# Kernel tuning notes

Hardware: AMD Instinct MI355X
Metric: run time of the kernel (lower is better)

Reference implementation:

```python
import jax, jax.numpy as jnp
import numpy as np

B, P, H, W, D, C = 16, 4, 32, 32, 32, 8


def setup_inputs() -> dict:
    key = jax.random.key(0)
    k1, k2 = jax.random.split(key)
    input_fmap = jax.random.normal(k1, (B, P, H, W, D, C), dtype=jnp.float32)
    # identity affine + small noise so sampled coords mostly stay in-volume
    ident = jnp.concatenate([jnp.eye(3, dtype=jnp.float32), jnp.zeros((3, 1), jnp.float32)], axis=1)
    theta = ident[None, None] + 0.05 * jax.random.normal(k2, (B, P, 3, 4), dtype=jnp.float32)
    return {"input_fmap": input_fmap, "theta": theta}


def _affine_grid(theta, H, W, D):
    # matches tf.meshgrid default 'xy' indexing: shapes (H, W, D)
    x = jnp.arange(W, dtype=jnp.float32)
    y = jnp.arange(H, dtype=jnp.float32)
    z = jnp.arange(D, dtype=jnp.float32)
    xt, yt, zt = jnp.meshgrid(x, y, z, indexing='xy')  # each (H, W, D)
    grid = jnp.stack([xt.ravel(), yt.ravel(), zt.ravel(), jnp.ones(H * W * D, jnp.float32)], axis=0)  # (4, HWD)
    bg = jnp.einsum('bpij,jn->bpin', theta, grid)  # (B, P, 3, HWD)
    return bg.reshape(theta.shape[0], theta.shape[1], 3, H, W, D)


def reference(input_fmap, theta):
    Bb, Pp, Hh, Ww, Dd, Cc = input_fmap.shape
    bg = _affine_grid(theta, Hh, Ww, Dd)
    x = bg[:, :, 0] + 2.0  # (B, P, H, W, D)
    y = bg[:, :, 1] + 2.0
    z = bg[:, :, 2] + 2.0
    padded = jnp.pad(input_fmap, ((0, 0), (0, 0), (2, 2), (2, 2), (2, 2), (0, 0)))
    # faithful to original: all three axes clipped with H+2 (cubic volume assumed)
    x0 = jnp.clip(jnp.floor(x).astype(jnp.int32), 0, Hh + 2)
    y0 = jnp.clip(jnp.floor(y).astype(jnp.int32), 0, Hh + 2)
    z0 = jnp.clip(jnp.floor(z).astype(jnp.int32), 0, Hh + 2)
    x1, y1, z1 = x0 + 1, y0 + 1, z0 + 1

    bi = jnp.arange(Bb)[:, None, None, None, None]
    pi = jnp.arange(Pp)[None, :, None, None, None]

    def gather(xi, yi, zi):
        # (B, P, H, W, D, C), indices applied to spatial dims with batch_dims=2
        return padded[bi, pi, xi, yi, zi]

    c000 = gather(x0, y0, z0)
    c001 = gather(x0, y0, z1)
    c010 = gather(x0, y1, z0)
    c011 = gather(x0, y1, z1)
    c100 = gather(x1, y0, z0)
    c101 = gather(x1, y0, z1)
    c110 = gather(x1, y1, z0)
    c111 = gather(x1, y1, z1)

    xd = (x - x0.astype(jnp.float32))[..., None]  # (B, P, H, W, D, 1)
    yd = (y - y0.astype(jnp.float32))[..., None]
    zd = (z - z0.astype(jnp.float32))[..., None]

    out = (c000 * (1 - xd) * (1 - yd) * (1 - zd)
           + c100 * xd * (1 - yd) * (1 - zd)
           + c010 * (1 - xd) * yd * (1 - zd)
           + c001 * (1 - xd) * (1 - yd) * zd
           + c101 * xd * (1 - yd) * zd
           + c011 * (1 - xd) * yd * zd
           + c110 * xd * yd * (1 - zd)
           + c111 * xd * yd * zd)
    return out
```

## Files before the change

kernel.cpp:

```cpp
#include <hip/hip_runtime.h>
#include <cstddef>

#define BB 16
#define PP 4
#define HH 32
#define WW 32
#define DD 32
#define CC 8

typedef float fx4 __attribute__((ext_vector_type(4)));

__global__ __launch_bounds__(256, 4) void resample_kernel(
    const float* __restrict__ fmap,
    const float* __restrict__ theta,
    float* __restrict__ out)
{
    const int g  = blockIdx.x * 256 + threadIdx.x;
    const int bp = g >> 15;
    const int r  = g & 32767;
    const int h  = r >> 10;
    const int w  = (r >> 5) & 31;
    const int d  = r & 31;

    const float* th = theta + bp * 12;
    const float t0 = th[0], t1 = th[1], t2  = th[2],  t3  = th[3];
    const float t4 = th[4], t5 = th[5], t6  = th[6],  t7  = th[7];
    const float t8 = th[8], t9 = th[9], t10 = th[10], t11 = th[11];

    const float fw = (float)w, fh = (float)h, fd = (float)d;
    const float x = fmaf(t0, fw, fmaf(t1, fh, fmaf(t2,  fd, t3 ))) + 2.0f;
    const float y = fmaf(t4, fw, fmaf(t5, fh, fmaf(t6,  fd, t7 ))) + 2.0f;
    const float z = fmaf(t8, fw, fmaf(t9, fh, fmaf(t10, fd, t11))) + 2.0f;

    const int x0 = min(max((int)floorf(x), 0), HH + 2);
    const int y0 = min(max((int)floorf(y), 0), HH + 2);
    const int z0 = min(max((int)floorf(z), 0), HH + 2);
    const float xd = x - (float)x0, yd = y - (float)y0, zd = z - (float)z0;

    const int ix[2] = { x0 - 2, x0 - 1 };
    const int iy[2] = { y0 - 2, y0 - 1 };
    const int iz[2] = { z0 - 2, z0 - 1 };
    const float wxv[2] = { (1.0f - xd) * (((unsigned)ix[0] < (unsigned)HH) ? 1.0f : 0.0f),
                           xd          * (((unsigned)ix[1] < (unsigned)HH) ? 1.0f : 0.0f) };
    const float wyv[2] = { (1.0f - yd) * (((unsigned)iy[0] < (unsigned)WW) ? 1.0f : 0.0f),
                           yd          * (((unsigned)iy[1] < (unsigned)WW) ? 1.0f : 0.0f) };
    const float wzv[2] = { (1.0f - zd) * (((unsigned)iz[0] < (unsigned)DD) ? 1.0f : 0.0f),
                           zd          * (((unsigned)iz[1] < (unsigned)DD) ? 1.0f : 0.0f) };
    const unsigned ox[2] = { (unsigned)(min(max(ix[0], 0), HH - 1) * (WW * DD * CC)),
                             (unsigned)(min(max(ix[1], 0), HH - 1) * (WW * DD * CC)) };
    const unsigned oy[2] = { (unsigned)(min(max(iy[0], 0), WW - 1) * (DD * CC)),
                             (unsigned)(min(max(iy[1], 0), WW - 1) * (DD * CC)) };
    const unsigned oz[2] = { (unsigned)(min(max(iz[0], 0), DD - 1) * CC),
                             (unsigned)(min(max(iz[1], 0), DD - 1) * CC) };

    const float* __restrict__ base = fmap + (size_t)bp * (HH * WW * DD * CC);

    unsigned voff[8];
    float    wgt[8];
    #pragma unroll
    for (int i = 0; i < 8; ++i) {
        const int bx = (i >> 2) & 1, by = (i >> 1) & 1, bz = i & 1;
        voff[i] = ox[bx] + oy[by] + oz[bz];
        wgt[i]  = wxv[bx] * wyv[by] * wzv[bz];
    }

    fx4 clo[8], chi[8];
    #pragma unroll
    for (int i = 0; i < 8; ++i) {
        clo[i] = *(const fx4*)(base + voff[i]);
        chi[i] = *(const fx4*)(base + voff[i] + 4);
    }
    __builtin_amdgcn_sched_barrier(0);

    fx4 alo = (fx4){0.f, 0.f, 0.f, 0.f};
    fx4 ahi = (fx4){0.f, 0.f, 0.f, 0.f};
    #pragma unroll
    for (int i = 0; i < 8; ++i) {
        const float gw = wgt[i];
        alo.x = fmaf(gw, clo[i].x, alo.x);
        alo.y = fmaf(gw, clo[i].y, alo.y);
        alo.z = fmaf(gw, clo[i].z, alo.z);
        alo.w = fmaf(gw, clo[i].w, alo.w);
        ahi.x = fmaf(gw, chi[i].x, ahi.x);
        ahi.y = fmaf(gw, chi[i].y, ahi.y);
        ahi.z = fmaf(gw, chi[i].z, ahi.z);
        ahi.w = fmaf(gw, chi[i].w, ahi.w);
    }

    float* o = out + (size_t)g * CC;
    __builtin_nontemporal_store(alo, (fx4*)o);
    __builtin_nontemporal_store(ahi, (fx4*)(o + 4));
}

extern "C" void kernel_launch(void* const* d_in, const int* in_sizes, int n_in,
                              void* d_out, int out_size, void* d_ws, size_t ws_size,
                              hipStream_t stream) {
    const float* fmap  = (const float*)d_in[0];
    const float* theta = (const float*)d_in[1];
    float* out = (float*)d_out;

    const int total_blocks = (BB * PP * HH * WW * DD) / 256;
    resample_kernel<<<dim3(total_blocks), dim3(256), 0, stream>>>(fmap, theta, out);
}
```

Baseline: 123.2 us.

## Split channels across thread pairs and software-pipeline gathers over persistent voxel chunks

Each pair of threads now shares one voxel, with each thread handling four channels. Each block processes 1024 voxels across 8 iterations and double-buffers the eight-corner gathers, so the next voxel's loads are in flight while the current one is accumulated and stored. Block indices are interleaved across chunks, and the h/d terms of the coordinates are hoisted out of the loop. This aims to hide gather latency and improve memory coalescing. In exchange, the grid is much smaller (2048 blocks), per-thread register use is higher, and the address math is duplicated across each thread pair.

```diff
diff --git a/kernel.cpp b/kernel.cpp
--- a/kernel.cpp
+++ b/kernel.cpp
@@ -8,6 +8,10 @@
 #define DD 32
 #define CC 8
 
+#define NBLK   2048
+#define ITERS  8
+#define VPI    128
+
 typedef float fx4 __attribute__((ext_vector_type(4)));
 
 __global__ __launch_bounds__(256, 4) void resample_kernel(
@@ -15,81 +19,100 @@
     const float* __restrict__ theta,
     float* __restrict__ out)
 {
-    const int g  = blockIdx.x * 256 + threadIdx.x;
-    const int bp = g >> 15;
-    const int r  = g & 32767;
-    const int h  = r >> 10;
-    const int w  = (r >> 5) & 31;
-    const int d  = r & 31;
+    const int tid  = threadIdx.x;
+    const int half = tid & 1;
+    const int vt   = tid >> 1;
+
+    const int chunk = (blockIdx.x & 7) * (NBLK / 8) + (blockIdx.x >> 3);
+    const int vox0  = chunk * (ITERS * VPI);
+
+    const int bp = vox0 >> 15;
+    const int h  = (vox0 & 32767) >> 10;
+    const int d  = vt & 31;
+    const int wb = vt >> 5;
 
     const float* th = theta + bp * 12;
     const float t0 = th[0], t1 = th[1], t2  = th[2],  t3  = th[3];
     const float t4 = th[4], t5 = th[5], t6  = th[6],  t7  = th[7];
     const float t8 = th[8], t9 = th[9], t10 = th[10], t11 = th[11];
 
-    const float fw = (float)w, fh = (float)h, fd = (float)d;
-    const float x = fmaf(t0, fw, fmaf(t1, fh, fmaf(t2,  fd, t3 ))) + 2.0f;
-    const float y = fmaf(t4, fw, fmaf(t5, fh, fmaf(t6,  fd, t7 ))) + 2.0f;
-    const float z = fmaf(t8, fw, fmaf(t9, fh, fmaf(t10, fd, t11))) + 2.0f;
+    const float fh = (float)h, fd = (float)d;
+    const float xb = fmaf(t1, fh, fmaf(t2,  fd, t3 )) + 2.0f;
+    const float yb = fmaf(t5, fh, fmaf(t6,  fd, t7 )) + 2.0f;
+    const float zb = fmaf(t9, fh, fmaf(t10, fd, t11)) + 2.0f;
 
-    const int x0 = min(max((int)floorf(x), 0), HH + 2);
-    const int y0 = min(max((int)floorf(y), 0), HH + 2);
-    const int z0 = min(max((int)floorf(z), 0), HH + 2);
-    const float xd = x - (float)x0, yd = y - (float)y0, zd = z - (float)z0;
+    const float* __restrict__ base =
+        fmap + (size_t)bp * (HH * WW * DD * CC) + half * 4;
 
-    const int ix[2] = { x0 - 2, x0 - 1 };
-    const int iy[2] = { y0 - 2, y0 - 1 };
-    const int iz[2] = { z0 - 2, z0 - 1 };
-    const float wxv[2] = { (1.0f - xd) * (((unsigned)ix[0] < (unsigned)HH) ? 1.0f : 0.0f),
-                           xd          * (((unsigned)ix[1] < (unsigned)HH) ? 1.0f : 0.0f) };
-    const float wyv[2] = { (1.0f - yd) * (((unsigned)iy[0] < (unsigned)WW) ? 1.0f : 0.0f),
-                           yd          * (((unsigned)iy[1] < (unsigned)WW) ? 1.0f : 0.0f) };
-    const float wzv[2] = { (1.0f - zd) * (((unsigned)iz[0] < (unsigned)DD) ? 1.0f : 0.0f),
-                           zd          * (((unsigned)iz[1] < (unsigned)DD) ? 1.0f : 0.0f) };
-    const unsigned ox[2] = { (unsigned)(min(max(ix[0], 0), HH - 1) * (WW * DD * CC)),
-                             (unsigned)(min(max(ix[1], 0), HH - 1) * (WW * DD * CC)) };
-    const unsigned oy[2] = { (unsigned)(min(max(iy[0], 0), WW - 1) * (DD * CC)),
-                             (unsigned)(min(max(iy[1], 0), WW - 1) * (DD * CC)) };
-    const unsigned oz[2] = { (unsigned)(min(max(iz[0], 0), DD - 1) * CC),
-                             (unsigned)(min(max(iz[1], 0), DD - 1) * CC) };
+    auto compute = [&](int j, unsigned* voff, float* wgt) {
+        const float fw = (float)(j * 4 + wb);
+        const float x = fmaf(t0, fw, xb);
+        const float y = fmaf(t4, fw, yb);
+        const float z = fmaf(t8, fw, zb);
 
-    const float* __restrict__ base = fmap + (size_t)bp * (HH * WW * DD * CC);
+        const int x0 = min(max((int)floorf(x), 0), HH + 2);
+        const int y0 = min(max((int)floorf(y), 0), HH + 2);
+        const int z0 = min(max((int)floorf(z), 0), HH + 2);
+        const float xd = x - (float)x0, yd = y - (float)y0, zd = z - (float)z0;
+
+        const int ix[2] = { x0 - 2, x0 - 1 };
+        const int iy[2] = { y0 - 2, y0 - 1 };
+        const int iz[2] = { z0 - 2, z0 - 1 };
+        const float wxv[2] = { (1.0f - xd) * (((unsigned)ix[0] < (unsigned)HH) ? 1.0f : 0.0f),
+                               xd          * (((unsigned)ix[1] < (unsigned)HH) ? 1.0f : 0.0f) };
+        const float wyv[2] = { (1.0f - yd) * (((unsigned)iy[0] < (unsigned)WW) ? 1.0f : 0.0f),
+                               yd          * (((unsigned)iy[1] < (unsigned)WW) ? 1.0f : 0.0f) };
+        const float wzv[2] = { (1.0f - zd) * (((unsigned)iz[0] < (unsigned)DD) ? 1.0f : 0.0f),
+                               zd          * (((unsigned)iz[1] < (unsigned)DD) ? 1.0f : 0.0f) };
+        const unsigned ox[2] = { (unsigned)(min(max(ix[0], 0), HH - 1) * (WW * DD * CC)),
+                                 (unsigned)(min(max(ix[1], 0), HH - 1) * (WW * DD * CC)) };
+        const unsigned oy[2] = { (unsigned)(min(max(iy[0], 0), WW - 1) * (DD * CC)),
+                                 (unsigned)(min(max(iy[1], 0), WW - 1) * (DD * CC)) };
+        const unsigned oz[2] = { (unsigned)(min(max(iz[0], 0), DD - 1) * CC),
+                                 (unsigned)(min(max(iz[1], 0), DD - 1) * CC) };
+        #pragma unroll
+        for (int i = 0; i < 8; ++i) {
+            const int bx = (i >> 2) & 1, by = (i >> 1) & 1, bz = i & 1;
+            voff[i] = ox[bx] + oy[by] + oz[bz];
+            wgt[i]  = wxv[bx] * wyv[by] * wzv[bz];
+        }
+    };
+
+    auto issue = [&](const unsigned* voff, fx4* c) {
+        #pragma unroll
+        for (int i = 0; i < 8; ++i)
+            c[i] = *(const fx4*)(base + voff[i]);
+    };
+
+    auto consume_store = [&](int j, const float* wgt, const fx4* c) {
+        fx4 acc = (fx4){0.f, 0.f, 0.f, 0.f};
+        #pragma unroll
+        for (int i = 0; i < 8; ++i) {
+            acc.x = fmaf(wgt[i], c[i].x, acc.x);
+            acc.y = fmaf(wgt[i], c[i].y, acc.y);
+            acc.z = fmaf(wgt[i], c[i].z, acc.z);
+            acc.w = fmaf(wgt[i], c[i].w, acc.w);
+        }
+        float* o = out + (size_t)(vox0 + j * VPI + vt) * CC + half * 4;
+        __builtin_nontemporal_store(acc, (fx4*)o);
+    };
 
     unsigned voff[8];
-    float    wgt[8];
+    float wgtA[8], wgtB[8];
+    fx4 cA[8], cB[8];
+
+    compute(0, voff, wgtA);
+    issue(voff, cA);
+
     #pragma unroll
-    for (int i = 0; i < 8; ++i) {
-        const int bx = (i >> 2) & 1, by = (i >> 1) & 1, bz = i & 1;
-        voff[i] = ox[bx] + oy[by] + oz[bz];
-        wgt[i]  = wxv[bx] * wyv[by] * wzv[bz];
+    for (int jj = 0; jj < ITERS; jj += 2) {
+        if (jj + 1 < ITERS) { compute(jj + 1, voff, wgtB); issue(voff, cB); }
+        __builtin_amdgcn_sched_barrier(0);
+        consume_store(jj, wgtA, cA);
+        if (jj + 2 < ITERS) { compute(jj + 2, voff, wgtA); issue(voff, cA); }
+        __builtin_amdgcn_sched_barrier(0);
+        consume_store(jj + 1, wgtB, cB);
     }
-
-    fx4 clo[8], chi[8];
-    #pragma unroll
-    for (int i = 0; i < 8; ++i) {
-        clo[i] = *(const fx4*)(base + voff[i]);
-        chi[i] = *(const fx4*)(base + voff[i] + 4);
-    }
-    __builtin_amdgcn_sched_barrier(0);
-
-    fx4 alo = (fx4){0.f, 0.f, 0.f, 0.f};
-    fx4 ahi = (fx4){0.f, 0.f, 0.f, 0.f};
-    #pragma unroll
-    for (int i = 0; i < 8; ++i) {
-        const float gw = wgt[i];
-        alo.x = fmaf(gw, clo[i].x, alo.x);
-        alo.y = fmaf(gw, clo[i].y, alo.y);
-        alo.z = fmaf(gw, clo[i].z, alo.z);
-        alo.w = fmaf(gw, clo[i].w, alo.w);
-        ahi.x = fmaf(gw, chi[i].x, ahi.x);
-        ahi.y = fmaf(gw, chi[i].y, ahi.y);
-        ahi.z = fmaf(gw, chi[i].z, ahi.z);
-        ahi.w = fmaf(gw, chi[i].w, ahi.w);
-    }
-
-    float* o = out + (size_t)g * CC;
-    __builtin_nontemporal_store(alo, (fx4*)o);
-    __builtin_nontemporal_store(ahi, (fx4*)(o + 4));
 }
 
 extern "C" void kernel_launch(void* const* d_in, const int* in_sizes, int n_in,
@@ -99,6 +122,5 @@
     const float* theta = (const float*)d_in[1];
     float* out = (float*)d_out;
 
-    const int total_blocks = (BB * PP * HH * WW * DD) / 256;
-    resample_kernel<<<dim3(total_blocks), dim3(256), 0, stream>>>(fmap, theta, out);
+    resample_kernel<<<dim3(NBLK), dim3(256), 0, stream>>>(fmap, theta, out);
 }
```

After: 126.1 us. 2.3% more time.

## Share z-neighbor corner loads across adjacent lanes via wave shuffles

Applied to the files above, without the earlier changes.

Each thread now loads only its four z0 corner voxels and, when the next lane's base cell is exactly one step further in z, takes that lane's loaded values through cross-lane shuffles as its z1 corners instead of issuing four more loads. Lanes where the condition fails load the z1 corners themselves. The aim is to halve global/L2 gather traffic and load instruction count. In exchange it adds 32 shuffle operations per thread plus selects, and the loads become divergent within a wave whenever some lanes need the fallback path.

```diff
diff --git a/kernel.cpp b/kernel.cpp
--- a/kernel.cpp
+++ b/kernel.cpp
@@ -15,12 +15,13 @@
     const float* __restrict__ theta,
     float* __restrict__ out)
 {
-    const int g  = blockIdx.x * 256 + threadIdx.x;
-    const int bp = g >> 15;
-    const int r  = g & 32767;
-    const int h  = r >> 10;
-    const int w  = (r >> 5) & 31;
-    const int d  = r & 31;
+    const int g    = blockIdx.x * 256 + threadIdx.x;
+    const int lane = threadIdx.x & 63;
+    const int bp   = g >> 15;
+    const int r    = g & 32767;
+    const int h    = r >> 10;
+    const int w    = (r >> 5) & 31;
+    const int d    = r & 31;
 
     const float* th = theta + bp * 12;
     const float t0 = th[0], t1 = th[1], t2  = th[2],  t3  = th[3];
@@ -50,41 +51,55 @@
                              (unsigned)(min(max(ix[1], 0), HH - 1) * (WW * DD * CC)) };
     const unsigned oy[2] = { (unsigned)(min(max(iy[0], 0), WW - 1) * (DD * CC)),
                              (unsigned)(min(max(iy[1], 0), WW - 1) * (DD * CC)) };
-    const unsigned oz[2] = { (unsigned)(min(max(iz[0], 0), DD - 1) * CC),
-                             (unsigned)(min(max(iz[1], 0), DD - 1) * CC) };
+    const unsigned ozA = (unsigned)(min(max(iz[0], 0), DD - 1) * CC);
+    const unsigned ozB = (unsigned)(min(max(iz[1], 0), DD - 1) * CC);
 
     const float* __restrict__ base = fmap + (size_t)bp * (HH * WW * DD * CC);
 
-    unsigned voff[8];
-    float    wgt[8];
+    const int pack    = (x0 << 12) | (y0 << 6) | z0;
+    const int nb_pack = __shfl(pack, lane + 1, 64);
+    const bool share  = (d != 31) && (nb_pack == pack + 1);
+
+    unsigned pxy[4];
+    fx4 Alo[4], Ahi[4], Blo[4], Bhi[4];
     #pragma unroll
-    for (int i = 0; i < 8; ++i) {
-        const int bx = (i >> 2) & 1, by = (i >> 1) & 1, bz = i & 1;
-        voff[i] = ox[bx] + oy[by] + oz[bz];
-        wgt[i]  = wxv[bx] * wyv[by] * wzv[bz];
+    for (int i = 0; i < 4; ++i) {
+        const int bx = i >> 1, by = i & 1;
+        pxy[i] = ox[bx] + oy[by];
+        Alo[i] = *(const fx4*)(base + pxy[i] + ozA);
+        Ahi[i] = *(const fx4*)(base + pxy[i] + ozA + 4);
     }
-
-    fx4 clo[8], chi[8];
-    #pragma unroll
-    for (int i = 0; i < 8; ++i) {
-        clo[i] = *(const fx4*)(base + voff[i]);
-        chi[i] = *(const fx4*)(base + voff[i] + 4);
+    if (!share) {
+        #pragma unroll
+        for (int i = 0; i < 4; ++i) {
+            Blo[i] = *(const fx4*)(base + pxy[i] + ozB);
+            Bhi[i] = *(const fx4*)(base + pxy[i] + ozB + 4);
+        }
     }
     __builtin_amdgcn_sched_barrier(0);
 
     fx4 alo = (fx4){0.f, 0.f, 0.f, 0.f};
     fx4 ahi = (fx4){0.f, 0.f, 0.f, 0.f};
     #pragma unroll
-    for (int i = 0; i < 8; ++i) {
-        const float gw = wgt[i];
-        alo.x = fmaf(gw, clo[i].x, alo.x);
-        alo.y = fmaf(gw, clo[i].y, alo.y);
-        alo.z = fmaf(gw, clo[i].z, alo.z);
-        alo.w = fmaf(gw, clo[i].w, alo.w);
-        ahi.x = fmaf(gw, chi[i].x, ahi.x);
-        ahi.y = fmaf(gw, chi[i].y, ahi.y);
-        ahi.z = fmaf(gw, chi[i].z, ahi.z);
-        ahi.w = fmaf(gw, chi[i].w, ahi.w);
+    for (int i = 0; i < 4; ++i) {
+        const int bx = i >> 1, by = i & 1;
+        const float wxy = wxv[bx] * wyv[by];
+        const float wA = wxy * wzv[0];
+        const float wB = wxy * wzv[1];
+
+        fx4 slo, shi;
+        #pragma unroll
+        for (int c = 0; c < 4; ++c) {
+            slo[c] = __shfl(Alo[i][c], lane + 1, 64);
+            shi[c] = __shfl(Ahi[i][c], lane + 1, 64);
+        }
+        #pragma unroll
+        for (int c = 0; c < 4; ++c) {
+            const float blo = share ? slo[c] : Blo[i][c];
+            const float bhi = share ? shi[c] : Bhi[i][c];
+            alo[c] = fmaf(wA, Alo[i][c], fmaf(wB, blo, alo[c]));
+            ahi[c] = fmaf(wA, Ahi[i][c], fmaf(wB, bhi, ahi[c]));
+        }
     }
 
     float* o = out + (size_t)g * CC;
```

After: 123.7 us. Within noise of the previous version (+0.4%).
